# Kernel optimization log

Hardware: AMD Instinct MI355X
Metric: run time of the kernel (lower is better)

Reference implementation:

```python
import jax, jax.numpy as jnp
import numpy as np

B, H, E, L = 2048, 4096, 8, 512
TAU = 1.0


def setup_inputs() -> dict:
    key = jax.random.key(0)
    k1, k2, k3, k4 = jax.random.split(key, 4)
    hidden = jax.random.normal(k1, (B, H), dtype=jnp.float32)
    envs = jax.random.normal(k2, (B, E), dtype=jnp.float32)
    idx = jnp.arange(B, dtype=jnp.int64)
    gumbel = jax.random.gumbel(k3, (B, E), dtype=jnp.float32)
    W = jax.random.normal(k4, (E, L, H), dtype=jnp.float32) * (1.0 / np.sqrt(H))
    return {"hidden": hidden, "envs": envs, "idx": idx, "gumbel": gumbel, "W": W}


def _hard_gumbel_softmax(log_probs, gumbel, tau):
    # F.gumbel_softmax(log_probs, tau=1, hard=True) with pre-sampled gumbel noise
    y_soft = jax.nn.softmax((log_probs + gumbel) / tau, axis=-1)
    y_hard = jax.nn.one_hot(jnp.argmax(y_soft, axis=-1), y_soft.shape[-1], dtype=y_soft.dtype)
    # straight-through estimator
    return y_hard + y_soft - jax.lax.stop_gradient(y_soft)


def reference(hidden, envs, idx, gumbel, W):
    # gating: env = gumbel_softmax(log_softmax(envs[idx]))  -> [B, E]
    log_probs = jax.nn.log_softmax(envs[idx], axis=-1)
    env = _hard_gumbel_softmax(log_probs, gumbel, TAU)
    # per-expert logits: [B, E, L]; fuses the per-sample python loop
    expert_logits = jnp.einsum("bh,elh->bel", hidden, W)
    # gating combine: [B, L]
    logits = jnp.einsum("be,bel->bl", env, expert_logits)
    # variance penalty over expert weights
    W_mean = jnp.mean(W, axis=0)  # [L, H]
    diff_sq = jnp.sum((W - W_mean[None]) ** 2, axis=(1, 2))  # ||W_e - W_mean||_2^2 per expert
    l1 = jnp.sum(jnp.abs(W), axis=(1, 2))                    # ||W_e||_1 per expert
    loss_penalty = jnp.mean(diff_sq / (l1 ** 2))
    return logits, loss_penalty
```

## Files before the change

### kernel.cpp

```cpp
#include <hip/hip_runtime.h>
#include <hip/hip_bf16.h>

constexpr int B = 2048, H = 4096, E = 8, L = 512;
constexpr int LH = L * H;

typedef float f4v __attribute__((ext_vector_type(4)));
typedef short short8 __attribute__((ext_vector_type(8)));

constexpr int BT = 128;
constexpr int LT = 128;
constexpr int KT = 32;
constexpr int SK = 4;
constexpr int RTMAX = 3;
constexpr int NITER = (H / SK) / KT;

constexpr int NGEMM = 4 * 2 * 4 * 4 * RTMAX;
constexpr int NPEN = 2048;

constexpr size_t WS_COUNTS = 0;
constexpr size_t WS_ACCUM = 32;
constexpr size_t WS_ROWLIST = 96;
constexpr size_t WS_ZERO_BYTES = 96;

using as1_u32 = const __attribute__((address_space(1))) unsigned int;
using as3_u32 = __attribute__((address_space(3))) unsigned int;

static __device__ __forceinline__ void dma16(const float* g, float* lds) {
  __builtin_amdgcn_global_load_lds((as1_u32*)g, (as3_u32*)lds, 16, 0, 0);
}

static __device__ __forceinline__ unsigned pk2(float a, float b) {
  __hip_bfloat162 p = __float22bfloat162_rn(make_float2(a, b));
  unsigned u;
  __builtin_memcpy(&u, &p, 4);
  return u;
}

static __device__ __forceinline__ short8 cvt8(f4v lo, f4v hi) {
  union { short8 s; unsigned u[4]; } r;
  r.u[0] = pk2(lo.x, lo.y);
  r.u[1] = pk2(lo.z, lo.w);
  r.u[2] = pk2(hi.x, hi.y);
  r.u[3] = pk2(hi.z, hi.w);
  return r.s;
}

__global__ void gating_kernel(const float* __restrict__ envs,
                              const float* __restrict__ gumbel,
                              int* __restrict__ counts,
                              int* __restrict__ row_list) {
  int b = blockIdx.x * blockDim.x + threadIdx.x;
  if (b >= B) return;
  float zmax = -1e30f;
  int am = 0;
#pragma unroll
  for (int e = 0; e < E; ++e) {
    float z = envs[b * E + e] + gumbel[b * E + e];
    if (z > zmax) { zmax = z; am = e; }
  }
  int pos = atomicAdd(&counts[am], 1);
  row_list[am * B + pos] = b;
}

__launch_bounds__(256, 2)
__global__ void fused_kernel(const float* __restrict__ hidden,
                             const float* __restrict__ W,
                             const int* __restrict__ counts,
                             const int* __restrict__ row_list,
                             float* __restrict__ out,
                             float* __restrict__ accum) {
  const int id = blockIdx.x;
  const int t = threadIdx.x;

  __shared__ __align__(16) float AshF[2][BT * KT];
  __shared__ __align__(16) float BshF[2][LT * KT];
  __shared__ int rlsh[BT];
  __shared__ float red[4][16];

  if (id >= NGEMM) {
    const int p = (id - NGEMM) * 256 + t;

    float4 w[E];
    float mx = 0.f, my = 0.f, mz = 0.f, mw = 0.f;
#pragma unroll
    for (int e = 0; e < E; ++e) {
      w[e] = *(const float4*)(W + (size_t)e * LH + (size_t)p * 4);
      mx += w[e].x; my += w[e].y; mz += w[e].z; mw += w[e].w;
    }
    mx *= 0.125f; my *= 0.125f; mz *= 0.125f; mw *= 0.125f;

    float vals[16];
#pragma unroll
    for (int e = 0; e < E; ++e) {
      float dx = w[e].x - mx, dy = w[e].y - my, dz = w[e].z - mz,
            dw = w[e].w - mw;
      vals[e] = dx * dx + dy * dy + dz * dz + dw * dw;
      vals[8 + e] =
          fabsf(w[e].x) + fabsf(w[e].y) + fabsf(w[e].z) + fabsf(w[e].w);
    }
#pragma unroll
    for (int k = 0; k < 16; ++k) {
      float v = vals[k];
      for (int off = 32; off > 0; off >>= 1) v += __shfl_xor(v, off);
      vals[k] = v;
    }
    const int wv = t >> 6, lane = t & 63;
    if (lane == 0) {
#pragma unroll
      for (int k = 0; k < 16; ++k) red[wv][k] = vals[k];
    }
    __syncthreads();
    if (t < 16) {
      atomicAdd(&accum[t], red[0][t] + red[1][t] + red[2][t] + red[3][t]);
    }
    return;
  }

  const int lt = id & 3;
  const int ep = (id >> 2) & 1;
  const int sk = (id >> 3) & 3;
  const int eh = (id >> 5) & 3;
  const int rt = id >> 7;
  const int e = eh * 2 + ep;

  const int cnt = counts[e];
  const int rbase = rt * BT;
  if (rbase >= cnt) return;
  const int lbase = lt * LT;

  if (t < BT) {
    int rr = rbase + t;
    rlsh[t] = row_list[e * B + (rr < cnt ? rr : (cnt - 1))];
  }
  __syncthreads();

  const float* Wp = W + (size_t)e * LH + (size_t)lbase * H;

  const int wave = t >> 6;
  const int lane = t & 63;
  const int quad = lane >> 4;
  const int l16 = lane & 15;
  const int wm = (wave >> 1) * 64;
  const int wn = (wave & 1) * 64;

  const int kbeg = sk * (H / SK);
  const int srow = lane >> 3;
  const int sblk = lane & 7;

  const float* sp[8];
  float* sl[2][8];
  const bool stageA = (wave < 2);
#pragma unroll
  for (int i = 0; i < 8; ++i) {
    int r = (stageA ? wave : (wave - 2)) * 64 + i * 8 + srow;
    int gblk = sblk ^ (r & 7);
    if (stageA) {
      sp[i] = hidden + (size_t)rlsh[r] * H + kbeg + gblk * 4;
      sl[0][i] = &AshF[0][(r - srow) * KT];
      sl[1][i] = &AshF[1][(r - srow) * KT];
    } else {
      sp[i] = Wp + (size_t)r * H + kbeg + gblk * 4;
      sl[0][i] = &BshF[0][(r - srow) * KT];
      sl[1][i] = &BshF[1][(r - srow) * KT];
    }
  }

  auto stage = [&](int buf) {
#pragma unroll
    for (int i = 0; i < 8; ++i) {
      dma16(sp[i], sl[buf][i]);
      sp[i] += KT;
    }
  };

  const int r7 = l16 & 7;
  const int slo = (2 * quad) ^ r7;
  const int shi = slo ^ 1;

  f4v acc[4][4] = {};

  stage(0);

  for (int it = 0; it < NITER; ++it) {
    const int buf = it & 1;
    __syncthreads();
    if (it + 1 < NITER) stage(buf ^ 1);

    short8 af[4], bf[4];
#pragma unroll
    for (int i = 0; i < 4; ++i) {
      int ra = wm + i * 16 + l16;
      f4v lo = *(const f4v*)&AshF[buf][ra * KT + slo * 4];
      f4v hi = *(const f4v*)&AshF[buf][ra * KT + shi * 4];
      af[i] = cvt8(lo, hi);
    }
#pragma unroll
    for (int j = 0; j < 4; ++j) {
      int rb = wn + j * 16 + l16;
      f4v lo = *(const f4v*)&BshF[buf][rb * KT + slo * 4];
      f4v hi = *(const f4v*)&BshF[buf][rb * KT + shi * 4];
      bf[j] = cvt8(lo, hi);
    }
#pragma unroll
    for (int i = 0; i < 4; ++i)
#pragma unroll
      for (int j = 0; j < 4; ++j)
        acc[i][j] =
            __builtin_amdgcn_mfma_f32_16x16x32_bf16(af[i], bf[j], acc[i][j],
                                                    0, 0, 0);
  }

#pragma unroll
  for (int i = 0; i < 4; ++i) {
#pragma unroll
    for (int j = 0; j < 4; ++j) {
#pragma unroll
      for (int reg = 0; reg < 4; ++reg) {
        int rloc = wm + i * 16 + quad * 4 + reg;
        if (rbase + rloc < cnt) {
          int bidx = rlsh[rloc];
          atomicAdd(&out[(size_t)bidx * L + lbase + wn + j * 16 + l16],
                    acc[i][j][reg]);
        }
      }
    }
  }
}

__global__ void finalize_kernel(const float* __restrict__ accum,
                                float* __restrict__ out) {
  if (threadIdx.x == 0) {
    float loss = 0.f;
#pragma unroll
    for (int e = 0; e < E; ++e) {
      float l1 = accum[8 + e];
      loss += accum[e] / (l1 * l1);
    }
    out[(size_t)B * L] = loss * 0.125f;
  }
}

extern "C" void kernel_launch(void* const* d_in, const int* in_sizes, int n_in,
                              void* d_out, int out_size, void* d_ws, size_t ws_size,
                              hipStream_t stream) {
  (void)in_sizes; (void)n_in; (void)ws_size;
  const float* hidden = (const float*)d_in[0];
  const float* envs   = (const float*)d_in[1];
  const float* gumbel = (const float*)d_in[3];
  const float* W      = (const float*)d_in[4];
  float* out = (float*)d_out;

  char* ws = (char*)d_ws;
  int*   counts   = (int*)(ws + WS_COUNTS);
  float* accum    = (float*)(ws + WS_ACCUM);
  int*   row_list = (int*)(ws + WS_ROWLIST);

  (void)hipMemsetAsync(d_ws, 0, WS_ZERO_BYTES, stream);
  (void)hipMemsetAsync(d_out, 0, (size_t)out_size * sizeof(float), stream);

  gating_kernel<<<dim3(B / 256), dim3(256), 0, stream>>>(envs, gumbel, counts,
                                                         row_list);

  fused_kernel<<<dim3(NGEMM + NPEN), dim3(256), 0, stream>>>(
      hidden, W, counts, row_list, out, accum);

  finalize_kernel<<<dim3(1), dim3(64), 0, stream>>>(accum, out);
}
```

Baseline: 184.3 us.

## Stage GEMM tiles as bf16 via registers, fold memsets and finalize into kernels

Result: slower. 225.7 us (+22.5%).

```diff
diff --git a/kernel.cpp b/kernel.cpp
--- a/kernel.cpp
+++ b/kernel.cpp
@@ -15,19 +15,13 @@
 constexpr int NITER = (H / SK) / KT;
 
 constexpr int NGEMM = 4 * 2 * 4 * 4 * RTMAX;
-constexpr int NPEN = 2048;
+constexpr int TPB = 512;
+constexpr int NPEN = (LH / 4) / TPB;
 
 constexpr size_t WS_COUNTS = 0;
 constexpr size_t WS_ACCUM = 32;
-constexpr size_t WS_ROWLIST = 96;
-constexpr size_t WS_ZERO_BYTES = 96;
-
-using as1_u32 = const __attribute__((address_space(1))) unsigned int;
-using as3_u32 = __attribute__((address_space(3))) unsigned int;
-
-static __device__ __forceinline__ void dma16(const float* g, float* lds) {
-  __builtin_amdgcn_global_load_lds((as1_u32*)g, (as3_u32*)lds, 16, 0, 0);
-}
+constexpr size_t WS_DONE = 96;
+constexpr size_t WS_ROWLIST = 128;
 
 static __device__ __forceinline__ unsigned pk2(float a, float b) {
   __hip_bfloat162 p = __float22bfloat162_rn(make_float2(a, b));
@@ -45,40 +39,77 @@
   return r.s;
 }
 
-__global__ void gating_kernel(const float* __restrict__ envs,
-                              const float* __restrict__ gumbel,
-                              int* __restrict__ counts,
-                              int* __restrict__ row_list) {
-  int b = blockIdx.x * blockDim.x + threadIdx.x;
-  if (b >= B) return;
-  float zmax = -1e30f;
-  int am = 0;
-#pragma unroll
-  for (int e = 0; e < E; ++e) {
-    float z = envs[b * E + e] + gumbel[b * E + e];
-    if (z > zmax) { zmax = z; am = e; }
-  }
-  int pos = atomicAdd(&counts[am], 1);
-  row_list[am * B + pos] = b;
-}
-
-__launch_bounds__(256, 2)
+static __device__ __forceinline__ void tile_barrier() {
+  asm volatile("s_waitcnt lgkmcnt(0)" ::: "memory");
+  __builtin_amdgcn_s_barrier();
+  asm volatile("" ::: "memory");
+}
+
+__global__ void prep_kernel(const float* __restrict__ envs,
+                            const float* __restrict__ gumbel,
+                            int* __restrict__ counts,
+                            float* __restrict__ accum,
+                            int* __restrict__ done,
+                            int* __restrict__ row_list,
+                            float* __restrict__ out) {
+  const int t = threadIdx.x;
+  const int id = blockIdx.x;
+  if (id < E) {
+    __shared__ int lcnt;
+    if (t == 0) lcnt = 0;
+    if (id == 0) {
+      if (t < 16) accum[t] = 0.f;
+      if (t == 16) *done = 0;
+    }
+    __syncthreads();
+#pragma unroll
+    for (int r = 0; r < 8; ++r) {
+      int b = r * 256 + t;
+      f4v e0 = *(const f4v*)(envs + b * E);
+      f4v e1 = *(const f4v*)(envs + b * E + 4);
+      f4v g0 = *(const f4v*)(gumbel + b * E);
+      f4v g1 = *(const f4v*)(gumbel + b * E + 4);
+      float z[8] = {e0.x + g0.x, e0.y + g0.y, e0.z + g0.z, e0.w + g0.w,
+                    e1.x + g1.x, e1.y + g1.y, e1.z + g1.z, e1.w + g1.w};
+      float zmax = z[0];
+      int am = 0;
+#pragma unroll
+      for (int e = 1; e < E; ++e)
+        if (z[e] > zmax) { zmax = z[e]; am = e; }
+      if (am == id) {
+        int pos = atomicAdd(&lcnt, 1);
+        row_list[id * B + pos] = b;
+      }
+    }
+    __syncthreads();
+    if (t == 0) counts[id] = lcnt;
+  } else {
+    const int cb = id - E;
+    f4v z = {0.f, 0.f, 0.f, 0.f};
+    f4v* dst = (f4v*)out + (size_t)cb * 1024;
+#pragma unroll
+    for (int i = 0; i < 4; ++i) dst[i * 256 + t] = z;
+  }
+}
+
+__launch_bounds__(TPB, 4)
 __global__ void fused_kernel(const float* __restrict__ hidden,
                              const float* __restrict__ W,
                              const int* __restrict__ counts,
                              const int* __restrict__ row_list,
                              float* __restrict__ out,
-                             float* __restrict__ accum) {
+                             float* __restrict__ accum,
+                             int* __restrict__ done) {
   const int id = blockIdx.x;
   const int t = threadIdx.x;
 
-  __shared__ __align__(16) float AshF[2][BT * KT];
-  __shared__ __align__(16) float BshF[2][LT * KT];
+  __shared__ __align__(16) short Ash[2][BT * KT];
+  __shared__ __align__(16) short Bsh[2][LT * KT];
   __shared__ int rlsh[BT];
-  __shared__ float red[4][16];
+  __shared__ float red[8][16];
 
   if (id >= NGEMM) {
-    const int p = (id - NGEMM) * 256 + t;
+    const int p = (id - NGEMM) * TPB + t;
 
     float4 w[E];
     float mx = 0.f, my = 0.f, mz = 0.f, mw = 0.f;
@@ -111,7 +142,27 @@
     }
     __syncthreads();
     if (t < 16) {
-      atomicAdd(&accum[t], red[0][t] + red[1][t] + red[2][t] + red[3][t]);
+      float s = red[0][t] + red[1][t] + red[2][t] + red[3][t] + red[4][t] +
+                red[5][t] + red[6][t] + red[7][t];
+      atomicAdd(&accum[t], s);
+      __threadfence();
+    }
+    __syncthreads();
+    if (t == 0) {
+      int prev = __hip_atomic_fetch_add(done, 1, __ATOMIC_ACQ_REL,
+                                        __HIP_MEMORY_SCOPE_AGENT);
+      if (prev == NPEN - 1) {
+        float loss = 0.f;
+#pragma unroll
+        for (int e = 0; e < E; ++e) {
+          float d = __hip_atomic_load(&accum[e], __ATOMIC_RELAXED,
+                                      __HIP_MEMORY_SCOPE_AGENT);
+          float l1 = __hip_atomic_load(&accum[8 + e], __ATOMIC_RELAXED,
+                                       __HIP_MEMORY_SCOPE_AGENT);
+          loss += d / (l1 * l1);
+        }
+        out[(size_t)B * L] = loss * 0.125f;
+      }
     }
     return;
   }
@@ -132,88 +183,90 @@
     int rr = rbase + t;
     rlsh[t] = row_list[e * B + (rr < cnt ? rr : (cnt - 1))];
   }
-  __syncthreads();
 
   const float* Wp = W + (size_t)e * LH + (size_t)lbase * H;
-
   const int wave = t >> 6;
   const int lane = t & 63;
   const int quad = lane >> 4;
   const int l16 = lane & 15;
-  const int wm = (wave >> 1) * 64;
-  const int wn = (wave & 1) * 64;
-
+  const int wm = (wave >> 2) * 64;
+  const int wn = (wave & 3) * 32;
   const int kbeg = sk * (H / SK);
-  const int srow = lane >> 3;
-  const int sblk = lane & 7;
-
-  const float* sp[8];
-  float* sl[2][8];
-  const bool stageA = (wave < 2);
-#pragma unroll
-  for (int i = 0; i < 8; ++i) {
-    int r = (stageA ? wave : (wave - 2)) * 64 + i * 8 + srow;
-    int gblk = sblk ^ (r & 7);
-    if (stageA) {
-      sp[i] = hidden + (size_t)rlsh[r] * H + kbeg + gblk * 4;
-      sl[0][i] = &AshF[0][(r - srow) * KT];
-      sl[1][i] = &AshF[1][(r - srow) * KT];
-    } else {
-      sp[i] = Wp + (size_t)r * H + kbeg + gblk * 4;
-      sl[0][i] = &BshF[0][(r - srow) * KT];
-      sl[1][i] = &BshF[1][(r - srow) * KT];
-    }
-  }
-
-  auto stage = [&](int buf) {
-#pragma unroll
-    for (int i = 0; i < 8; ++i) {
-      dma16(sp[i], sl[buf][i]);
-      sp[i] += KT;
-    }
+
+  const bool stA = (wave < 4);
+  const int srow0 = (wave & 3) * 32 + (lane >> 2);
+  const int srow1 = srow0 + 16;
+  const int c16 = lane & 3;
+
+  tile_barrier();
+
+  const float *p0, *p1;
+  if (stA) {
+    p0 = hidden + (size_t)rlsh[srow0] * H + kbeg + c16 * 8;
+    p1 = hidden + (size_t)rlsh[srow1] * H + kbeg + c16 * 8;
+  } else {
+    p0 = Wp + (size_t)srow0 * H + kbeg + c16 * 8;
+    p1 = Wp + (size_t)srow1 * H + kbeg + c16 * 8;
+  }
+  short* ld0base = stA ? &Ash[0][0] : &Bsh[0][0];
+  short* ld1base = stA ? &Ash[1][0] : &Bsh[1][0];
+  const int ldo0 = srow0 * KT + c16 * 8;
+  const int ldo1 = srow1 * KT + c16 * 8;
+
+  f4v ga0, ga1, ga2, ga3;
+  f4v gb0, gb1, gb2, gb3;
+
+  auto issue = [&](f4v& x0, f4v& x1, f4v& x2, f4v& x3) {
+    x0 = *(const f4v*)p0;
+    x1 = *(const f4v*)(p0 + 4);
+    x2 = *(const f4v*)p1;
+    x3 = *(const f4v*)(p1 + 4);
+    p0 += KT;
+    p1 += KT;
   };
-
-  const int r7 = l16 & 7;
-  const int slo = (2 * quad) ^ r7;
-  const int shi = slo ^ 1;
-
-  f4v acc[4][4] = {};
-
-  stage(0);
-
-  for (int it = 0; it < NITER; ++it) {
-    const int buf = it & 1;
-    __syncthreads();
-    if (it + 1 < NITER) stage(buf ^ 1);
-
-    short8 af[4], bf[4];
-#pragma unroll
-    for (int i = 0; i < 4; ++i) {
-      int ra = wm + i * 16 + l16;
-      f4v lo = *(const f4v*)&AshF[buf][ra * KT + slo * 4];
-      f4v hi = *(const f4v*)&AshF[buf][ra * KT + shi * 4];
-      af[i] = cvt8(lo, hi);
-    }
-#pragma unroll
-    for (int j = 0; j < 4; ++j) {
-      int rb = wn + j * 16 + l16;
-      f4v lo = *(const f4v*)&BshF[buf][rb * KT + slo * 4];
-      f4v hi = *(const f4v*)&BshF[buf][rb * KT + shi * 4];
-      bf[j] = cvt8(lo, hi);
-    }
+  auto store2 = [&](short* base, f4v x0, f4v x1, f4v x2, f4v x3) {
+    *(short8*)(base + ldo0) = cvt8(x0, x1);
+    *(short8*)(base + ldo1) = cvt8(x2, x3);
+  };
+
+  f4v acc[4][2] = {};
+  auto compute = [&](int bufc) {
+    short8 af[4], bf[2];
 #pragma unroll
     for (int i = 0; i < 4; ++i)
-#pragma unroll
-      for (int j = 0; j < 4; ++j)
-        acc[i][j] =
-            __builtin_amdgcn_mfma_f32_16x16x32_bf16(af[i], bf[j], acc[i][j],
-                                                    0, 0, 0);
+      af[i] = *(const short8*)&Ash[bufc][(wm + i * 16 + l16) * KT + quad * 8];
+#pragma unroll
+    for (int j = 0; j < 2; ++j)
+      bf[j] = *(const short8*)&Bsh[bufc][(wn + j * 16 + l16) * KT + quad * 8];
+#pragma unroll
+    for (int i = 0; i < 4; ++i)
+#pragma unroll
+      for (int j = 0; j < 2; ++j)
+        acc[i][j] = __builtin_amdgcn_mfma_f32_16x16x32_bf16(af[i], bf[j],
+                                                            acc[i][j], 0, 0, 0);
+  };
+
+  issue(ga0, ga1, ga2, ga3);
+  issue(gb0, gb1, gb2, gb3);
+  store2(ld0base, ga0, ga1, ga2, ga3);
+  tile_barrier();
+
+  for (int it2 = 0; it2 < NITER / 2; ++it2) {
+    const bool more = (it2 + 1 < NITER / 2);
+    if (more) issue(ga0, ga1, ga2, ga3);
+    compute(0);
+    store2(ld1base, gb0, gb1, gb2, gb3);
+    tile_barrier();
+    if (more) issue(gb0, gb1, gb2, gb3);
+    compute(1);
+    if (more) store2(ld0base, ga0, ga1, ga2, ga3);
+    tile_barrier();
   }
 
 #pragma unroll
   for (int i = 0; i < 4; ++i) {
 #pragma unroll
-    for (int j = 0; j < 4; ++j) {
+    for (int j = 0; j < 2; ++j) {
 #pragma unroll
       for (int reg = 0; reg < 4; ++reg) {
         int rloc = wm + i * 16 + quad * 4 + reg;
@@ -227,23 +280,10 @@
   }
 }
 
-__global__ void finalize_kernel(const float* __restrict__ accum,
-                                float* __restrict__ out) {
-  if (threadIdx.x == 0) {
-    float loss = 0.f;
-#pragma unroll
-    for (int e = 0; e < E; ++e) {
-      float l1 = accum[8 + e];
-      loss += accum[e] / (l1 * l1);
-    }
-    out[(size_t)B * L] = loss * 0.125f;
-  }
-}
-
 extern "C" void kernel_launch(void* const* d_in, const int* in_sizes, int n_in,
-                              void* d_out, int out_size, void* d_ws, size_t ws_size,
-                              hipStream_t stream) {
-  (void)in_sizes; (void)n_in; (void)ws_size;
+                              void* d_out, int out_size, void* d_ws,
+                              size_t ws_size, hipStream_t stream) {
+  (void)in_sizes; (void)n_in; (void)ws_size; (void)out_size;
   const float* hidden = (const float*)d_in[0];
   const float* envs   = (const float*)d_in[1];
   const float* gumbel = (const float*)d_in[3];
@@ -253,16 +293,12 @@
   char* ws = (char*)d_ws;
   int*   counts   = (int*)(ws + WS_COUNTS);
   float* accum    = (float*)(ws + WS_ACCUM);
+  int*   done     = (int*)(ws + WS_DONE);
   int*   row_list = (int*)(ws + WS_ROWLIST);
 
-  (void)hipMemsetAsync(d_ws, 0, WS_ZERO_BYTES, stream);
-  (void)hipMemsetAsync(d_out, 0, (size_t)out_size * sizeof(float), stream);
-
-  gating_kernel<<<dim3(B / 256), dim3(256), 0, stream>>>(envs, gumbel, counts,
-                                                         row_list);
-
-  fused_kernel<<<dim3(NGEMM + NPEN), dim3(256), 0, stream>>>(
-      hidden, W, counts, row_list, out, accum);
-
-  finalize_kernel<<<dim3(1), dim3(64), 0, stream>>>(accum, out);
-}
+  prep_kernel<<<dim3(E + 256), dim3(256), 0, stream>>>(envs, gumbel, counts,
+                                                       accum, done, row_list,
+                                                       out);
+  fused_kernel<<<dim3(NGEMM + NPEN), dim3(TPB), 0, stream>>>(
+      hidden, W, counts, row_list, out, accum, done);
+}
```
